# Kernel tuning notes

Hardware: AMD Instinct MI355X
Metric: run time of the kernel (lower is better)

## Reference

```python
import jax, jax.numpy as jnp
import numpy as np

N_NODES = 50000
N_EDGES = 1600000
DIM_IN = 128
DIM_OUT = 128
EPS = 1e-10


def setup_inputs() -> dict:
    key = jax.random.key(0)
    k1, k2, k3, k4, k5 = jax.random.split(key, 5)
    feat_in = jax.random.normal(k1, (N_NODES, DIM_IN), dtype=jnp.float32)
    rows = jax.random.randint(k2, (N_EDGES,), 0, N_NODES, dtype=jnp.int32)
    cols = jax.random.randint(k3, (N_EDGES,), 0, N_NODES, dtype=jnp.int32)
    # normalized adjacency values (positive, ~1/deg scale)
    vals = jax.random.uniform(k4, (N_EDGES,), dtype=jnp.float32) / 32.0
    W = jax.random.normal(k5, (DIM_OUT, DIM_IN), dtype=jnp.float32) * 0.05
    b = jnp.zeros((DIM_OUT,), dtype=jnp.float32)
    scale = jnp.ones((DIM_OUT,), dtype=jnp.float32)
    offset = jnp.zeros((DIM_OUT,), dtype=jnp.float32)
    return {"feat_in": feat_in, "rows": rows, "cols": cols, "vals": vals,
            "W": W, "b": b, "scale": scale, "offset": offset}


def reference(feat_in, rows, cols, vals, W, b, scale, offset):
    # torch.sparse.mm(adj_norm, feat_in): gather source features, scale by
    # edge value, scatter-add into destination rows.
    msgs = vals[:, None] * feat_in[cols]                       # [E, D_in]
    feat_aggr = jax.ops.segment_sum(msgs, rows, num_segments=N_NODES)  # [N, D_in]
    # f_lin (nn.Linear): x @ W.T + b
    feat_trans = feat_aggr @ W.T + b                           # [N, D_out]
    # act = ReLU
    a = jax.nn.relu(feat_trans)
    # f_norm: per-row (feature-dim) normalization, biased variance
    mean = jnp.mean(a, axis=1, keepdims=True)
    var = jnp.mean((a - mean) ** 2, axis=1, keepdims=True) + EPS
    feat_out = (a - mean) * scale * jax.lax.rsqrt(var) + offset
    return feat_out
```

## Files before the change

kernel.cpp:

```cpp
#include <hip/hip_runtime.h>

typedef unsigned int uint;
typedef unsigned short ushort;
typedef __attribute__((ext_vector_type(8))) short short8;
typedef __attribute__((ext_vector_type(4))) float floatx4;

#define N_NODES 50000
#define N_EDGES 1600000
#define DIM 128
#define LN_EPS 1e-10f

#define ROWS_PER_BUCKET 64
#define N_BUCKETS 782
#define BUCKET_CAP 2560
#define EPB 6250
#define SB 256
#define FCB 1563
#define CAPR 76

__device__ __forceinline__ uint f2bf(float x) {
    uint u = __float_as_uint(x);
    return (u + 0x7FFFu + ((u >> 16) & 1u)) >> 16;
}

__global__ __launch_bounds__(1024) void prep(
    const float* __restrict__ feat, const float* __restrict__ W,
    const int* __restrict__ rows, const int* __restrict__ cols,
    const float* __restrict__ vals, int* __restrict__ gcnt,
    int2* __restrict__ perm, uint* __restrict__ featb_u,
    ushort* __restrict__ wbf)
{
    __shared__ int  cnt[N_BUCKETS];
    __shared__ int  gbase[N_BUCKETS];
    __shared__ int  lbase[N_BUCKETS];
    __shared__ int  csum[64];
    __shared__ uint stash[EPB];
    __shared__ int2 stageE[EPB];
    const int bx = blockIdx.x;
    const int t  = threadIdx.x;

    if (bx >= SB) {
        int cb = bx - SB;
        if (cb < FCB) {
            int i = cb * 1024 + t;
            if (i < N_NODES * DIM / 4) {
                float4 v = ((const float4*)feat)[i];
                ((uint2*)featb_u)[i] = make_uint2(
                    f2bf(v.x) | (f2bf(v.y) << 16),
                    f2bf(v.z) | (f2bf(v.w) << 16));
            }
        } else {
            for (int idx = t; idx < DIM * DIM; idx += 1024)
                wbf[idx] = (ushort)f2bf(W[idx]);
        }
        return;
    }

    for (int i = t; i < N_BUCKETS; i += 1024) cnt[i] = 0;
    __syncthreads();
    const int base = bx * EPB;
    for (int k = t; k < EPB; k += 1024) {
        int r = rows[base + k];
        int rank = atomicAdd(&cnt[r >> 6], 1);
        stash[k] = ((uint)rank << 16) | (uint)r;
    }
    __syncthreads();

    for (int i = t; i < N_BUCKETS; i += 1024) {
        int c = cnt[i];
        gbase[i] = c ? atomicAdd(&gcnt[i], c) : 0;
    }
    if (t < 64) {
        int s = 0;
        for (int j = 0; j < 13; ++j) {
            int idx = t * 13 + j;
            if (idx < N_BUCKETS) s += cnt[idx];
        }
        csum[t] = s;
    }
    __syncthreads();
    if (t == 0) {
        int s = 0;
        for (int i = 0; i < 64; ++i) { int c = csum[i]; csum[i] = s; s += c; }
    }
    __syncthreads();
    if (t < 64) {
        int run = csum[t];
        for (int j = 0; j < 13; ++j) {
            int idx = t * 13 + j;
            if (idx < N_BUCKETS) { lbase[idx] = run; run += cnt[idx]; }
        }
    }
    __syncthreads();

    for (int k = t; k < EPB; k += 1024) {
        int e = base + k;
        uint s = stash[k];
        int r = (int)(s & 0xFFFFu);
        int rank = (int)(s >> 16);
        int b = r >> 6;
        int pos = lbase[b] + rank;
        stageE[pos] = make_int2(
            (uint)cols[e] | ((uint)(r & 63) << 16) | ((uint)b << 22),
            __float_as_int(vals[e]));
    }
    __syncthreads();

    for (int j = t; j < EPB; j += 1024) {
        int2 p = stageE[j];
        uint b = ((uint)p.x) >> 22;
        int pos = gbase[b] + (j - lbase[b]);
        if (pos < BUCKET_CAP)
            perm[(size_t)b * BUCKET_CAP + pos] = p;
    }
}

__global__ __launch_bounds__(512, 6) void agg_fused(
    const int2* __restrict__ perm, const int* __restrict__ gcnt,
    const ushort* __restrict__ featb, const ushort* __restrict__ wbf,
    const float* __restrict__ bias, const float* __restrict__ scale,
    const float* __restrict__ offset, float* __restrict__ out)
{
    __shared__ int2 lists[32 * CAPR];
    ushort* rowsbuf = (ushort*)lists;
    float*  Cbuf    = (float*)lists;
    __shared__ int  lcnt[32];

    const int t = threadIdx.x;
    const int b  = blockIdx.x >> 1;
    const int lo = (blockIdx.x & 1) * 32;
    if (t < 32) lcnt[t] = 0;
    __syncthreads();

    int n = gcnt[b];
    if (n > BUCKET_CAP) n = BUCKET_CAP;
    const int2* pb = perm + (size_t)b * BUCKET_CAP;

    for (int e = t; e < n; e += 512) {
        int2 p = pb[e];
        int rl = ((p.x >> 16) & 63) - lo;
        if ((uint)rl < 32u) {
            int pos = atomicAdd(&lcnt[rl], 1);
            if (pos < CAPR)
                lists[rl * CAPR + pos] = make_int2(p.x & 0xFFFF, p.y);
        }
    }
    __syncthreads();

    const int lane = t & 63;
    const int wid  = t >> 6;
    const int rb   = wid * 4;

    float ax[4], ay[4];
    #pragma unroll
    for (int j = 0; j < 4; ++j) {
        int rl = rb + j;
        int cnt = lcnt[rl];
        if (cnt > CAPR) cnt = CAPR;
        const int2* L = &lists[rl * CAPR];
        float sx = 0.f, sy = 0.f;
        int e = 0;
        for (; e + 7 < cnt; e += 8) {
            int2 p[8]; uint g[8];
            #pragma unroll
            for (int k = 0; k < 8; ++k) p[k] = L[e + k];
            #pragma unroll
            for (int k = 0; k < 8; ++k)
                g[k] = ((const uint*)(featb + (size_t)p[k].x * DIM))[lane];
            #pragma unroll
            for (int k = 0; k < 8; ++k) {
                float v = __int_as_float(p[k].y);
                sx = fmaf(v, __uint_as_float(g[k] << 16), sx);
                sy = fmaf(v, __uint_as_float(g[k] & 0xFFFF0000u), sy);
            }
        }
        for (; e < cnt; ++e) {
            int2 p = L[e];
            uint g = ((const uint*)(featb + (size_t)p.x * DIM))[lane];
            float v = __int_as_float(p.y);
            sx = fmaf(v, __uint_as_float(g << 16), sx);
            sy = fmaf(v, __uint_as_float(g & 0xFFFF0000u), sy);
        }
        ax[j] = sx; ay[j] = sy;
    }
    __syncthreads();

    #pragma unroll
    for (int j = 0; j < 4; ++j) {
        uint pk = f2bf(ax[j]) | (f2bf(ay[j]) << 16);
        *(uint*)&rowsbuf[(rb + j) * 136 + 2 * lane] = pk;
    }
    __syncthreads();

    const int l15  = lane & 15;
    const int quad = lane >> 4;
    const int n0   = wid * 16 + l15;
    const float bb = bias[n0];

    floatx4 acc0 = {0.f, 0.f, 0.f, 0.f};
    floatx4 acc1 = {0.f, 0.f, 0.f, 0.f};
    #pragma unroll
    for (int kt = 0; kt < 4; ++kt) {
        int k0 = kt * 32 + quad * 8;
        short8 af0 = *(const short8*)&rowsbuf[l15 * 136 + k0];
        short8 af1 = *(const short8*)&rowsbuf[(l15 + 16) * 136 + k0];
        short8 bf  = *(const short8*)&wbf[n0 * DIM + k0];
        acc0 = __builtin_amdgcn_mfma_f32_16x16x32_bf16(af0, bf, acc0, 0, 0, 0);
        acc1 = __builtin_amdgcn_mfma_f32_16x16x32_bf16(af1, bf, acc1, 0, 0, 0);
    }
    __syncthreads();

    #pragma unroll
    for (int r = 0; r < 4; ++r) {
        int m = quad * 4 + r;
        Cbuf[m * 132 + n0]        = acc0[r] + bb;
        Cbuf[(m + 16) * 132 + n0] = acc1[r] + bb;
    }
    __syncthreads();

    const float sc0 = scale[lane],  sc1 = scale[lane + 64];
    const float of0 = offset[lane], of1 = offset[lane + 64];

    #pragma unroll
    for (int j = 0; j < 4; ++j) {
        int rl = rb + j;
        int r  = b * ROWS_PER_BUCKET + lo + rl;
        if (r >= N_NODES) continue;
        float A0 = fmaxf(Cbuf[rl * 132 + lane],      0.0f);
        float A1 = fmaxf(Cbuf[rl * 132 + lane + 64], 0.0f);

        float s = A0 + A1;
        #pragma unroll
        for (int off = 32; off >= 1; off >>= 1) s += __shfl_xor(s, off, 64);
        float mean = s * (1.0f / 128.0f);

        float d0 = A0 - mean, d1 = A1 - mean;
        float q = d0 * d0 + d1 * d1;
        #pragma unroll
        for (int off = 32; off >= 1; off >>= 1) q += __shfl_xor(q, off, 64);
        float rstd = rsqrtf(q * (1.0f / 128.0f) + LN_EPS);

        size_t rowp = (size_t)r * DIM;
        out[rowp + lane]      = d0 * sc0 * rstd + of0;
        out[rowp + lane + 64] = d1 * sc1 * rstd + of1;
    }
}

extern "C" void kernel_launch(void* const* d_in, const int* in_sizes, int n_in,
                              void* d_out, int out_size, void* d_ws, size_t ws_size,
                              hipStream_t stream) {
    const float* feat_in = (const float*)d_in[0];
    const int*   rows    = (const int*)d_in[1];
    const int*   cols    = (const int*)d_in[2];
    const float* vals    = (const float*)d_in[3];
    const float* W       = (const float*)d_in[4];
    const float* bias    = (const float*)d_in[5];
    const float* scale   = (const float*)d_in[6];
    const float* offset  = (const float*)d_in[7];
    float* out = (float*)d_out;

    char* p = (char*)d_ws;
    int2* perm = (int2*)p;                 p += (size_t)N_BUCKETS * BUCKET_CAP * 8;
    ushort* featb = (ushort*)p;            p += (size_t)N_NODES * DIM * 2;
    ushort* wbf = (ushort*)p;              p += DIM * DIM * 2;
    int*  gcnt = (int*)p;                  p += (size_t)(N_BUCKETS + 64) * 4;

    hipMemsetAsync(gcnt, 0, (size_t)N_BUCKETS * sizeof(int), stream);

    prep<<<SB + FCB + 1, 1024, 0, stream>>>(feat_in, W, rows, cols, vals,
                                            gcnt, perm, (uint*)featb, wbf);
    agg_fused<<<N_BUCKETS * 2, 512, 0, stream>>>(perm, gcnt, featb, wbf,
                                                 bias, scale, offset, out);
}
```

Before: 176.8 us.

## Rebalance prep grid, remap blocks across XCDs, and precompute gather byte offsets

```diff
diff --git a/kernel.cpp b/kernel.cpp
--- a/kernel.cpp
+++ b/kernel.cpp
@@ -13,9 +13,9 @@
 #define ROWS_PER_BUCKET 64
 #define N_BUCKETS 782
 #define BUCKET_CAP 2560
-#define EPB 6250
-#define SB 256
-#define FCB 1563
+#define SB 512
+#define EPB 3125
+#define CONVB 512
 #define CAPR 76
 
 __device__ __forceinline__ uint f2bf(float x) {
@@ -23,7 +23,7 @@
     return (u + 0x7FFFu + ((u >> 16) & 1u)) >> 16;
 }
 
-__global__ __launch_bounds__(1024) void prep(
+__global__ __launch_bounds__(512) void scatter(
     const float* __restrict__ feat, const float* __restrict__ W,
     const int* __restrict__ rows, const int* __restrict__ cols,
     const float* __restrict__ vals, int* __restrict__ gcnt,
@@ -40,33 +40,35 @@
     const int t  = threadIdx.x;
 
     if (bx >= SB) {
-        int cb = bx - SB;
-        if (cb < FCB) {
-            int i = cb * 1024 + t;
-            if (i < N_NODES * DIM / 4) {
-                float4 v = ((const float4*)feat)[i];
-                ((uint2*)featb_u)[i] = make_uint2(
-                    f2bf(v.x) | (f2bf(v.y) << 16),
-                    f2bf(v.z) | (f2bf(v.w) << 16));
-            }
-        } else {
-            for (int idx = t; idx < DIM * DIM; idx += 1024)
-                wbf[idx] = (ushort)f2bf(W[idx]);
+        const int cb = bx - SB;
+        const int stride = CONVB * 512;
+        for (int i = cb * 512 + t; i < N_NODES * DIM / 4; i += stride) {
+            float4 v = ((const float4*)feat)[i];
+            ((uint2*)featb_u)[i] = make_uint2(
+                f2bf(v.x) | (f2bf(v.y) << 16),
+                f2bf(v.z) | (f2bf(v.w) << 16));
+        }
+        for (int i = cb * 512 + t; i < DIM * DIM / 4; i += stride) {
+            float4 v = ((const float4*)W)[i];
+            ushort4 o;
+            o.x = (ushort)f2bf(v.x); o.y = (ushort)f2bf(v.y);
+            o.z = (ushort)f2bf(v.z); o.w = (ushort)f2bf(v.w);
+            ((ushort4*)wbf)[i] = o;
         }
         return;
     }
 
-    for (int i = t; i < N_BUCKETS; i += 1024) cnt[i] = 0;
+    for (int i = t; i < N_BUCKETS; i += 512) cnt[i] = 0;
     __syncthreads();
     const int base = bx * EPB;
-    for (int k = t; k < EPB; k += 1024) {
+    for (int k = t; k < EPB; k += 512) {
         int r = rows[base + k];
         int rank = atomicAdd(&cnt[r >> 6], 1);
         stash[k] = ((uint)rank << 16) | (uint)r;
     }
     __syncthreads();
 
-    for (int i = t; i < N_BUCKETS; i += 1024) {
+    for (int i = t; i < N_BUCKETS; i += 512) {
         int c = cnt[i];
         gbase[i] = c ? atomicAdd(&gcnt[i], c) : 0;
     }
@@ -93,7 +95,7 @@
     }
     __syncthreads();
 
-    for (int k = t; k < EPB; k += 1024) {
+    for (int k = t; k < EPB; k += 512) {
         int e = base + k;
         uint s = stash[k];
         int r = (int)(s & 0xFFFFu);
@@ -106,7 +108,7 @@
     }
     __syncthreads();
 
-    for (int j = t; j < EPB; j += 1024) {
+    for (int j = t; j < EPB; j += 512) {
         int2 p = stageE[j];
         uint b = ((uint)p.x) >> 22;
         int pos = gbase[b] + (j - lbase[b]);
@@ -127,8 +129,14 @@
     __shared__ int  lcnt[32];
 
     const int t = threadIdx.x;
-    const int b  = blockIdx.x >> 1;
-    const int lo = (blockIdx.x & 1) * 32;
+
+    const int nwg = N_BUCKETS * 2;
+    const int q = nwg >> 3, rr = nwg & 7;
+    const int xcd = blockIdx.x & 7, within = blockIdx.x >> 3;
+    const int w = (xcd < rr ? xcd * (q + 1) : rr * (q + 1) + (xcd - rr) * q) + within;
+    const int b  = w >> 1;
+    const int lo = (w & 1) * 32;
+
     if (t < 32) lcnt[t] = 0;
     __syncthreads();
 
@@ -142,7 +150,7 @@
         if ((uint)rl < 32u) {
             int pos = atomicAdd(&lcnt[rl], 1);
             if (pos < CAPR)
-                lists[rl * CAPR + pos] = make_int2(p.x & 0xFFFF, p.y);
+                lists[rl * CAPR + pos] = make_int2((p.x & 0xFFFF) << 8, p.y);
         }
     }
     __syncthreads();
@@ -150,6 +158,8 @@
     const int lane = t & 63;
     const int wid  = t >> 6;
     const int rb   = wid * 4;
+    const char* fbase = (const char*)featb;
+    const uint  lane4 = (uint)lane << 2;
 
     float ax[4], ay[4];
     #pragma unroll
@@ -166,7 +176,7 @@
             for (int k = 0; k < 8; ++k) p[k] = L[e + k];
             #pragma unroll
             for (int k = 0; k < 8; ++k)
-                g[k] = ((const uint*)(featb + (size_t)p[k].x * DIM))[lane];
+                g[k] = *(const uint*)(fbase + ((uint)p[k].x + lane4));
             #pragma unroll
             for (int k = 0; k < 8; ++k) {
                 float v = __int_as_float(p[k].y);
@@ -176,7 +186,7 @@
         }
         for (; e < cnt; ++e) {
             int2 p = L[e];
-            uint g = ((const uint*)(featb + (size_t)p.x * DIM))[lane];
+            uint g = *(const uint*)(fbase + ((uint)p.x + lane4));
             float v = __int_as_float(p.y);
             sx = fmaf(v, __uint_as_float(g << 16), sx);
             sy = fmaf(v, __uint_as_float(g & 0xFFFF0000u), sy);
@@ -235,10 +245,10 @@
         float mean = s * (1.0f / 128.0f);
 
         float d0 = A0 - mean, d1 = A1 - mean;
-        float q = d0 * d0 + d1 * d1;
+        float q2 = d0 * d0 + d1 * d1;
         #pragma unroll
-        for (int off = 32; off >= 1; off >>= 1) q += __shfl_xor(q, off, 64);
-        float rstd = rsqrtf(q * (1.0f / 128.0f) + LN_EPS);
+        for (int off = 32; off >= 1; off >>= 1) q2 += __shfl_xor(q2, off, 64);
+        float rstd = rsqrtf(q2 * (1.0f / 128.0f) + LN_EPS);
 
         size_t rowp = (size_t)r * DIM;
         out[rowp + lane]      = d0 * sc0 * rstd + of0;
@@ -267,7 +277,7 @@
 
     hipMemsetAsync(gcnt, 0, (size_t)N_BUCKETS * sizeof(int), stream);
 
-    prep<<<SB + FCB + 1, 1024, 0, stream>>>(feat_in, W, rows, cols, vals,
+    scatter<<<SB + CONVB, 512, 0, stream>>>(feat_in, W, rows, cols, vals,
                                             gcnt, perm, (uint*)featb, wbf);
     agg_fused<<<N_BUCKETS * 2, 512, 0, stream>>>(perm, gcnt, featb, wbf,
                                                  bias, scale, offset, out);
```

Measured after the change: 181.8 us. 1.03x slower.
